# Kernel optimization log

Hardware: AMD Instinct MI355X
Metric: run time of the kernel (lower is better)

The kernel has to match this reference:

```python
import jax, jax.numpy as jnp
import numpy as np

B, N, E, H = 1, 4096, 1024, 16
D = E // H

def setup_inputs() -> dict:
    key = jax.random.key(0)
    k1, k2, k3 = jax.random.split(key, 3)
    s = 1.0 / np.sqrt(E)
    return {
        "x": jax.random.normal(k1, (B, N, E), dtype=jnp.float32),
        "w_qkv": jax.random.normal(k2, (3 * E, E), dtype=jnp.float32) * s,
        "b_qkv": jnp.zeros((3 * E,), dtype=jnp.float32),
        "w_proj": jax.random.normal(k3, (E, E), dtype=jnp.float32) * s,
        "b_proj": jnp.zeros((E,), dtype=jnp.float32),
    }

def reference(x, w_qkv, b_qkv, w_proj, b_proj):
    Bx, Nx, Ex = x.shape
    scale = (Ex // H) ** -0.5
    # torch Linear: x @ W^T + b
    qkv = jnp.einsum('bne,fe->bnf', x, w_qkv) + b_qkv  # [B,N,3E]
    q, k, v = jnp.split(qkv, 3, axis=-1)
    def to_heads(t):
        return t.reshape(Bx, Nx, H, Ex // H).transpose(0, 2, 1, 3)  # b h n d
    q, k, v = to_heads(q), to_heads(k), to_heads(v)
    dots = jnp.einsum('bhnd,bhmd->bhnm', q, k) * scale  # full NxN scores
    attn = jax.nn.softmax(dots, axis=-1)  # dropout=0 (eval)
    out = jnp.einsum('bhnm,bhmd->bhnd', attn, v)
    out = out.transpose(0, 2, 1, 3).reshape(Bx, Nx, Ex)
    return jnp.einsum('bne,fe->bnf', out, w_proj) + b_proj
```

## Files before the change

kernel.cpp:

```cpp
#include <hip/hip_runtime.h>

#define N_TOK 4096
#define E_DIM 1024
#define NH    16
#define HD    64

typedef __bf16 bf16x8 __attribute__((ext_vector_type(8)));
typedef __bf16 bf16x4 __attribute__((ext_vector_type(4)));
typedef float  f32x4  __attribute__((ext_vector_type(4)));
typedef float  f32x16 __attribute__((ext_vector_type(16)));

#define GLOAD16(gsrc, ldst) __builtin_amdgcn_global_load_lds( \
    (const __attribute__((address_space(1))) void*)(gsrc),    \
    (__attribute__((address_space(3))) void*)(ldst), 16, 0, 0)

__device__ __forceinline__ f32x16 zero16() {
    f32x16 z;
#pragma unroll
    for (int i = 0; i < 16; ++i) z[i] = 0.f;
    return z;
}

__device__ __forceinline__ unsigned pk2(float a, float b) {
    union { __bf16 h[2]; unsigned u; } t;
    t.h[0] = (__bf16)a; t.h[1] = (__bf16)b;
    return t.u;
}

__device__ __forceinline__ float fmax3(float a, float b, float c) {
    return fmaxf(fmaxf(a, b), c);
}

__device__ __forceinline__ void load16(const __bf16* __restrict__ p, bf16x8& lo, bf16x8& hi) {
    lo = *(const bf16x8*)p;
    hi = *(const bf16x8*)(p + 8);
}

__device__ __forceinline__ void cvt8(const float* __restrict__ src, __bf16* __restrict__ dst, int i) {
    const float4 a = ((const float4*)src)[i * 2];
    const float4 b = ((const float4*)src)[i * 2 + 1];
    ((bf16x8*)dst)[i] = bf16x8{(__bf16)a.x, (__bf16)a.y, (__bf16)a.z, (__bf16)a.w,
                               (__bf16)b.x, (__bf16)b.y, (__bf16)b.z, (__bf16)b.w};
}

__global__ __launch_bounds__(256) void conv_tri(const float* __restrict__ s1, __bf16* __restrict__ d1, int n1,
                                                const float* __restrict__ s2, __bf16* __restrict__ d2, int n2,
                                                const float* __restrict__ s3, __bf16* __restrict__ d3, int n3) {
    const int i = blockIdx.x * 256 + threadIdx.x;
    if (i < n1)                 cvt8(s1, d1, i);
    else if (i < n1 + n2)       cvt8(s2, d2, i - n1);
    else if (i < n1 + n2 + n3)  cvt8(s3, d3, i - n1 - n2);
}

__global__ __launch_bounds__(256) void conv_pair(const float* __restrict__ s1, __bf16* __restrict__ d1, int n1,
                                                 const float* __restrict__ s2, __bf16* __restrict__ d2, int n2) {
    const int i = blockIdx.x * 256 + threadIdx.x;
    if (i < n1)            cvt8(s1, d1, i);
    else if (i < n1 + n2)  cvt8(s2, d2, i - n1);
}

__global__ __launch_bounds__(256) void conv_bf16(const float* __restrict__ src,
                                                 __bf16* __restrict__ dst, int n8) {
    const int i = blockIdx.x * 256 + threadIdx.x;
    if (i >= n8) return;
    cvt8(src, dst, i);
}

__device__ __forceinline__ void gemm_core(const __bf16* __restrict__ A, const __bf16* __restrict__ B,
                                          const int K, const int rowBase, const int colBase,
                                          __bf16* As, __bf16* Bs, f32x4 (&acc)[4][4]) {
    const int tid = threadIdx.x, lane = tid & 63, wid = tid >> 6;
    const int wm = wid >> 1, wn = wid & 1;
    const int lr = lane & 15, lg = lane >> 4;
    const int lrow = lane >> 2, lcol = (lane & 3) * 8;

    const __bf16* aBase = A + (size_t)(rowBase + wid * 16 + lrow) * K + lcol;
    const __bf16* bBase = B + (size_t)(colBase + wid * 16 + lrow) * K + lcol;
    const size_t row64 = (size_t)64 * K;

    for (int kt = 0; kt < K; kt += 32) {
        __syncthreads();
        GLOAD16(aBase + kt,         As + wid * 512);
        GLOAD16(aBase + row64 + kt, As + 2048 + wid * 512);
        GLOAD16(bBase + kt,         Bs + wid * 512);
        GLOAD16(bBase + row64 + kt, Bs + 2048 + wid * 512);
        __syncthreads();

        bf16x8 af[4], bfr[4];
#pragma unroll
        for (int i = 0; i < 4; ++i) {
            af[i]  = *(const bf16x8*)&As[(wm * 64 + i * 16 + lr) * 32 + lg * 8];
            bfr[i] = *(const bf16x8*)&Bs[(wn * 64 + i * 16 + lr) * 32 + lg * 8];
        }
#pragma unroll
        for (int i = 0; i < 4; ++i)
#pragma unroll
            for (int j = 0; j < 4; ++j)
                acc[i][j] = __builtin_amdgcn_mfma_f32_16x16x32_bf16(af[i], bfr[j], acc[i][j], 0, 0, 0);
    }
}

#define QSCALE 0.180336879f

__global__ __launch_bounds__(256) void qkv_gemm(const __bf16* __restrict__ x,
                                                const __bf16* __restrict__ wqkv,
                                                const float* __restrict__ bqkv,
                                                __bf16* __restrict__ Qb,
                                                __bf16* __restrict__ Kb,
                                                __bf16* __restrict__ VtG) {
    __shared__ __bf16 As[128 * 32];
    __shared__ __bf16 Bs[128 * 32];
    f32x4 acc[4][4];
#pragma unroll
    for (int i = 0; i < 4; ++i)
#pragma unroll
        for (int j = 0; j < 4; ++j)
            acc[i][j] = f32x4{0.f, 0.f, 0.f, 0.f};

    const int lin = blockIdx.y * 32 + blockIdx.x;
    const int swz = (lin & 7) * 96 + (lin >> 3);
    const int tm = swz & 31, tn = swz >> 5;

    gemm_core(x, wqkv, E_DIM, tm * 128, tn * 128, As, Bs, acc);

    const int tid = threadIdx.x;
    const int lane = tid & 63, wid = tid >> 6;
    const int wm = wid >> 1, wn = wid & 1;
    const int lr = lane & 15, lg = lane >> 4;

#pragma unroll
    for (int ni = 0; ni < 4; ++ni) {
        const int f = tn * 128 + wn * 64 + ni * 16 + lr;
        const float bias = bqkv[f];
        const int which = f >> 10;
        const int hh = (f & 1023) >> 6;
        const int dd = f & 63;
        if (which == 2) {
            __bf16* dst = VtG + ((size_t)hh * HD + dd) * N_TOK;
#pragma unroll
            for (int mi = 0; mi < 4; ++mi) {
                const int n0 = tm * 128 + wm * 64 + mi * 16 + lg * 4;
                const int pos = (n0 & ~12) | ((n0 & 4) << 1) | ((n0 & 8) >> 1);
                bf16x4 v;
#pragma unroll
                for (int r = 0; r < 4; ++r) v[r] = (__bf16)(acc[mi][ni][r] + bias);
                *(bf16x4*)&dst[pos] = v;
            }
        } else {
            __bf16* dst = (which == 0) ? Qb : Kb;
            const float sc = (which == 0) ? QSCALE : 1.0f;
#pragma unroll
            for (int mi = 0; mi < 4; ++mi) {
#pragma unroll
                for (int r = 0; r < 4; ++r) {
                    const int n = tm * 128 + wm * 64 + mi * 16 + lg * 4 + r;
                    dst[((size_t)hh * N_TOK + n) * HD + dd] = (__bf16)((acc[mi][ni][r] + bias) * sc);
                }
            }
        }
    }
}

#define QBLK  256
#define KVB   128
#define NTILE (N_TOK / KVB)
#define KST   72
#define VST   136
#define BUFSZ (KVB * KST + HD * VST)

__global__ __launch_bounds__(512, 2) void flash_attn(const __bf16* __restrict__ Qb,
                                                     const __bf16* __restrict__ Kb,
                                                     const __bf16* __restrict__ Vt,
                                                     __bf16* __restrict__ Ob) {
    __shared__ __bf16 smem[2 * BUFSZ];

    const int tid = threadIdx.x, lane = tid & 63, wid = tid >> 6;
    const int lq = lane & 31, hi = lane >> 5;
    const int qg = wid >> 1, hw = wid & 1;

    const int lin = blockIdx.y * 16 + blockIdx.x;
    const int swz = (lin & 7) * 32 + (lin >> 3);
    const int qblk = swz & 15, h = swz >> 4;

    const __bf16* Qh = Qb + (size_t)h * N_TOK * HD;
    const __bf16* Kh = Kb + (size_t)h * N_TOK * HD;
    const __bf16* Vh = Vt + (size_t)h * HD * N_TOK;

    bf16x8 qf[2][4];
#pragma unroll
    for (int g = 0; g < 2; ++g) {
        const size_t qr = (size_t)qblk * QBLK + qg * 64 + g * 32 + lq;
#pragma unroll
        for (int sd = 0; sd < 4; ++sd)
            qf[g][sd] = *(const bf16x8*)&Qh[qr * HD + sd * 16 + hi * 8];
    }

    f32x16 o[2][2], lacc[2];
#pragma unroll
    for (int g = 0; g < 2; ++g) { o[g][0] = zero16(); o[g][1] = zero16(); lacc[g] = zero16(); }
    float m[2] = {-INFINITY, -INFINITY};

    const bf16x8 ones = bf16x8{(__bf16)1.f, (__bf16)1.f, (__bf16)1.f, (__bf16)1.f,
                               (__bf16)1.f, (__bf16)1.f, (__bf16)1.f, (__bf16)1.f};

    const int krow = tid >> 2, kseg = (tid & 3) * 16;
    const int vrow = tid >> 3, vseg = (tid & 7) * 16;
    const __bf16* kSrc = Kh + (size_t)krow * HD + kseg;
    const __bf16* vSrc = Vh + (size_t)vrow * N_TOK + vseg;

    bf16x8 kr0, kr1, vr0, vr1;
    load16(kSrc, kr0, kr1);
    load16(vSrc, vr0, vr1);
    {
        __bf16* Kw = smem;
        __bf16* Vw = smem + KVB * KST;
        *(bf16x8*)&Kw[krow * KST + kseg]     = kr0;
        *(bf16x8*)&Kw[krow * KST + kseg + 8] = kr1;
        *(bf16x8*)&Vw[vrow * VST + vseg]     = vr0;
        *(bf16x8*)&Vw[vrow * VST + vseg + 8] = vr1;
    }

    for (int t = 0; t < NTILE; ++t) {
        const int cur = t & 1;
        const __bf16* Kc = smem + cur * BUFSZ;
        const __bf16* Vc = Kc + KVB * KST;

        if (t + 1 < NTILE) {
            load16(kSrc + (size_t)(t + 1) * KVB * HD, kr0, kr1);
            load16(vSrc + (t + 1) * KVB, vr0, vr1);
        }
        __syncthreads();

        f32x16 s[2][2];
#pragma unroll
        for (int g = 0; g < 2; ++g) { s[g][0] = zero16(); s[g][1] = zero16(); }
        __builtin_amdgcn_s_setprio(1);
#pragma unroll
        for (int sd = 0; sd < 4; ++sd) {
            const bf16x8 kf0 = *(const bf16x8*)&Kc[(hw * 64 + lq) * KST + sd * 16 + hi * 8];
            const bf16x8 kf1 = *(const bf16x8*)&Kc[(hw * 64 + 32 + lq) * KST + sd * 16 + hi * 8];
            s[0][0] = __builtin_amdgcn_mfma_f32_32x32x16_bf16(kf0, qf[0][sd], s[0][0], 0, 0, 0);
            s[0][1] = __builtin_amdgcn_mfma_f32_32x32x16_bf16(kf1, qf[0][sd], s[0][1], 0, 0, 0);
            s[1][0] = __builtin_amdgcn_mfma_f32_32x32x16_bf16(kf0, qf[1][sd], s[1][0], 0, 0, 0);
            s[1][1] = __builtin_amdgcn_mfma_f32_32x32x16_bf16(kf1, qf[1][sd], s[1][1], 0, 0, 0);
        }
        __builtin_amdgcn_s_setprio(0);

        float mx[2];
#pragma unroll
        for (int g = 0; g < 2; ++g) {
            const float t0 = fmax3(s[g][0][0],  s[g][0][1],  s[g][0][2]);
            const float t1 = fmax3(s[g][0][3],  s[g][0][4],  s[g][0][5]);
            const float t2 = fmax3(s[g][0][6],  s[g][0][7],  s[g][0][8]);
            const float t3 = fmax3(s[g][0][9],  s[g][0][10], s[g][0][11]);
            const float t4 = fmax3(s[g][0][12], s[g][0][13], s[g][0][14]);
            const float t5 = fmax3(s[g][1][0],  s[g][1][1],  s[g][1][2]);
            const float t6 = fmax3(s[g][1][3],  s[g][1][4],  s[g][1][5]);
            const float t7 = fmax3(s[g][1][6],  s[g][1][7],  s[g][1][8]);
            const float t8 = fmax3(s[g][1][9],  s[g][1][10], s[g][1][11]);
            const float t9 = fmax3(s[g][1][12], s[g][1][13], s[g][1][14]);
            const float u0 = fmax3(t0, t1, s[g][0][15]);
            const float u1 = fmax3(t2, t3, t4);
            const float u2 = fmax3(t5, t6, s[g][1][15]);
            const float u3 = fmax3(t7, t8, t9);
            float a = fmaxf(fmax3(u0, u1, u2), u3);
            mx[g] = fmaxf(a, __shfl_xor(a, 32));
        }

        if (!__all(mx[0] <= m[0] + 8.f && mx[1] <= m[1] + 8.f)) {
#pragma unroll
            for (int g = 0; g < 2; ++g) {
                const float mn = fmaxf(m[g], mx[g]);
                const float al = __builtin_amdgcn_exp2f(m[g] - mn);
                m[g] = mn;
#pragma unroll
                for (int r = 0; r < 16; ++r) { o[g][0][r] *= al; o[g][1][r] *= al; }
                lacc[g][0] *= al;
            }
        }

#pragma unroll
        for (int w = 0; w < 4; ++w) {
            const int rb = (w & 1) * 8;
            const int half = (w < 2) ? 0 : 1;
            bf16x8 pfv[2];
#pragma unroll
            for (int g = 0; g < 2; ++g) {
                union { unsigned u[4]; bf16x8 v; } pf;
                pf.u[0] = pk2(__builtin_amdgcn_exp2f(s[g][half][rb + 0] - m[g]),
                              __builtin_amdgcn_exp2f(s[g][half][rb + 1] - m[g]));
                pf.u[1] = pk2(__builtin_amdgcn_exp2f(s[g][half][rb + 2] - m[g]),
                              __builtin_amdgcn_exp2f(s[g][half][rb + 3] - m[g]));
                pf.u[2] = pk2(__builtin_amdgcn_exp2f(s[g][half][rb + 4] - m[g]),
                              __builtin_amdgcn_exp2f(s[g][half][rb + 5] - m[g]));
                pf.u[3] = pk2(__builtin_amdgcn_exp2f(s[g][half][rb + 6] - m[g]),
                              __builtin_amdgcn_exp2f(s[g][half][rb + 7] - m[g]));
                pfv[g] = pf.v;
            }

            const bf16x8 vf0 = *(const bf16x8*)&Vc[lq * VST + hw * 64 + w * 16 + hi * 8];
            const bf16x8 vf1 = *(const bf16x8*)&Vc[(32 + lq) * VST + hw * 64 + w * 16 + hi * 8];
            __builtin_amdgcn_s_setprio(1);
            o[0][0] = __builtin_amdgcn_mfma_f32_32x32x16_bf16(vf0, pfv[0], o[0][0], 0, 0, 0);
            o[0][1] = __builtin_amdgcn_mfma_f32_32x32x16_bf16(vf1, pfv[0], o[0][1], 0, 0, 0);
            o[1][0] = __builtin_amdgcn_mfma_f32_32x32x16_bf16(vf0, pfv[1], o[1][0], 0, 0, 0);
            o[1][1] = __builtin_amdgcn_mfma_f32_32x32x16_bf16(vf1, pfv[1], o[1][1], 0, 0, 0);
            lacc[0] = __builtin_amdgcn_mfma_f32_32x32x16_bf16(ones, pfv[0], lacc[0], 0, 0, 0);
            lacc[1] = __builtin_amdgcn_mfma_f32_32x32x16_bf16(ones, pfv[1], lacc[1], 0, 0, 0);
            __builtin_amdgcn_s_setprio(0);
        }

        if (t + 1 < NTILE) {
            __bf16* Kw = smem + (cur ^ 1) * BUFSZ;
            __bf16* Vw = Kw + KVB * KST;
            *(bf16x8*)&Kw[krow * KST + kseg]     = kr0;
            *(bf16x8*)&Kw[krow * KST + kseg + 8] = kr1;
            *(bf16x8*)&Vw[vrow * VST + vseg]     = vr0;
            *(bf16x8*)&Vw[vrow * VST + vseg + 8] = vr1;
        }
    }

    __syncthreads();
    float* scratch = (float*)smem;
    if (hw == 1) {
#pragma unroll
        for (int g = 0; g < 2; ++g) {
            float* po = scratch + (qg * 2 + g) * 2080;
#pragma unroll
            for (int r = 0; r < 16; ++r) {
                const int d0 = (r & 3) + 8 * (r >> 2) + 4 * hi;
                po[lq * 65 + d0]      = o[g][0][r];
                po[lq * 65 + 32 + d0] = o[g][1][r];
            }
            if (hi == 0) {
                float* plm = scratch + 16640 + (qg * 2 + g) * 64;
                plm[lq * 2] = lacc[g][0]; plm[lq * 2 + 1] = m[g];
            }
        }
    }
    __syncthreads();
    if (hw == 0) {
#pragma unroll
        for (int g = 0; g < 2; ++g) {
            float* po  = scratch + (qg * 2 + g) * 2080;
            float* plm = scratch + 16640 + (qg * 2 + g) * 64;
            const float l1 = plm[lq * 2], m1 = plm[lq * 2 + 1];
            const float M  = fmaxf(m[g], m1);
            const float a0 = __builtin_amdgcn_exp2f(m[g] - M);
            const float a1 = __builtin_amdgcn_exp2f(m1 - M);
            const float inv = 1.0f / (lacc[g][0] * a0 + l1 * a1);
            const size_t qr = (size_t)qblk * QBLK + qg * 64 + g * 32 + lq;
            __bf16* obase = &Ob[qr * E_DIM + h * HD];
#pragma unroll
            for (int grp = 0; grp < 4; ++grp) {
                bf16x4 v0, v1;
#pragma unroll
                for (int c = 0; c < 4; ++c) {
                    const int r = grp * 4 + c;
                    const int d0 = c + 8 * grp + 4 * hi;
                    v0[c] = (__bf16)((o[g][0][r] * a0 + po[lq * 65 + d0]      * a1) * inv);
                    v1[c] = (__bf16)((o[g][1][r] * a0 + po[lq * 65 + 32 + d0] * a1) * inv);
                }
                *(bf16x4*)&obase[grp * 8 + hi * 4]      = v0;
                *(bf16x4*)&obase[32 + grp * 8 + hi * 4] = v1;
            }
        }
    }
}

__global__ __launch_bounds__(256) void proj_gemm(const __bf16* __restrict__ Ob,
                                                 const __bf16* __restrict__ wp,
                                                 const float* __restrict__ bp,
                                                 float* __restrict__ out) {
    __shared__ __bf16 As[64 * 32];
    __shared__ __bf16 Bs[128 * 32];
    f32x4 acc[2][4];
#pragma unroll
    for (int i = 0; i < 2; ++i)
#pragma unroll
        for (int j = 0; j < 4; ++j)
            acc[i][j] = f32x4{0.f, 0.f, 0.f, 0.f};

    const int lin = blockIdx.y * 64 + blockIdx.x;
    const int swz = (lin & 7) * 64 + (lin >> 3);
    const int tm = swz & 63, tn = swz >> 6;

    const int tid = threadIdx.x, lane = tid & 63, wid = tid >> 6;
    const int wm = wid >> 1, wn = wid & 1;
    const int lr = lane & 15, lg = lane >> 4;
    const int lrow = lane >> 2, lcol = (lane & 3) * 8;

    const __bf16* aBase = Ob + (size_t)(tm * 64 + wid * 16 + lrow) * E_DIM + lcol;
    const __bf16* bBase = wp + (size_t)(tn * 128 + wid * 16 + lrow) * E_DIM + lcol;
    const size_t row64 = (size_t)64 * E_DIM;

    for (int kt = 0; kt < E_DIM; kt += 32) {
        __syncthreads();
        GLOAD16(aBase + kt,         As + wid * 512);
        GLOAD16(bBase + kt,         Bs + wid * 512);
        GLOAD16(bBase + row64 + kt, Bs + 2048 + wid * 512);
        __syncthreads();

        bf16x8 af[2], bfr[4];
#pragma unroll
        for (int i = 0; i < 2; ++i)
            af[i]  = *(const bf16x8*)&As[(wm * 32 + i * 16 + lr) * 32 + lg * 8];
#pragma unroll
        for (int j = 0; j < 4; ++j)
            bfr[j] = *(const bf16x8*)&Bs[(wn * 64 + j * 16 + lr) * 32 + lg * 8];
#pragma unroll
        for (int i = 0; i < 2; ++i)
#pragma unroll
            for (int j = 0; j < 4; ++j)
                acc[i][j] = __builtin_amdgcn_mfma_f32_16x16x32_bf16(af[i], bfr[j], acc[i][j], 0, 0, 0);
    }

#pragma unroll
    for (int ni = 0; ni < 4; ++ni) {
        const int f = tn * 128 + wn * 64 + ni * 16 + lr;
        const float bias = bp[f];
#pragma unroll
        for (int mi = 0; mi < 2; ++mi) {
#pragma unroll
            for (int r = 0; r < 4; ++r) {
                const int n = tm * 64 + wm * 32 + mi * 16 + lg * 4 + r;
                out[(size_t)n * E_DIM + f] = acc[mi][ni][r] + bias;
            }
        }
    }
}

extern "C" void kernel_launch(void* const* d_in, const int* in_sizes, int n_in,
                              void* d_out, int out_size, void* d_ws, size_t ws_size,
                              hipStream_t stream) {
    const float* x     = (const float*)d_in[0];
    const float* wqkv  = (const float*)d_in[1];
    const float* bqkv  = (const float*)d_in[2];
    const float* wproj = (const float*)d_in[3];
    const float* bproj = (const float*)d_in[4];
    float* out = (float*)d_out;

    const size_t headElems = (size_t)NH * N_TOK * HD;
    __bf16* Qb   = (__bf16*)d_ws;
    __bf16* Kb   = Qb + headElems;
    __bf16* VtG  = Kb + headElems;
    __bf16* ObXb = VtG + headElems;
    __bf16* Wb   = ObXb + headElems;

    const int n1 = N_TOK * E_DIM / 8;
    const int n2 = 3 * E_DIM * E_DIM / 8;
    const int n3 = E_DIM * E_DIM / 8;

    const size_t needBytes = (4 * headElems + (size_t)(3 + 1) * E_DIM * E_DIM) * sizeof(__bf16);
    const bool sep = ws_size >= needBytes;
    __bf16* Wp = sep ? (Wb + (size_t)3 * E_DIM * E_DIM) : Wb;

    if (sep) {
        conv_tri<<<(n1 + n2 + n3 + 255) / 256, 256, 0, stream>>>(x, ObXb, n1, wqkv, Wb, n2, wproj, Wp, n3);
    } else {
        conv_pair<<<(n1 + n2 + 255) / 256, 256, 0, stream>>>(x, ObXb, n1, wqkv, Wb, n2);
    }

    qkv_gemm<<<dim3(N_TOK / 128, 3 * E_DIM / 128), 256, 0, stream>>>(ObXb, Wb, bqkv, Qb, Kb, VtG);

    if (!sep) {
        conv_bf16<<<(n3 + 255) / 256, 256, 0, stream>>>(wproj, Wp, n3);
    }

    flash_attn<<<dim3(N_TOK / QBLK, NH), 512, 0, stream>>>(Qb, Kb, VtG, ObXb);

    proj_gemm<<<dim3(N_TOK / 64, E_DIM / 128), 256, 0, stream>>>(ObXb, Wp, bproj, out);
}
```

Baseline: 153.2 us.

## Load K/V fragments directly from global memory instead of LDS staging

Removes the double-buffered LDS staging of K and V tiles and the per-tile __syncthreads in the flash attention loop. Each wave now reads its K and V MFMA fragments straight from global memory into registers, so there is no barrier and no LDS round-trip. The cost is that the four query-group waves sharing the same K/V rows now fetch them redundantly through cache, and without software prefetch the loads are exposed latency. There is also added register pressure under launch_bounds(512,2).

```diff
diff --git a/kernel.cpp b/kernel.cpp
--- a/kernel.cpp
+++ b/kernel.cpp
@@ -29,11 +29,6 @@
 
 __device__ __forceinline__ float fmax3(float a, float b, float c) {
     return fmaxf(fmaxf(a, b), c);
-}
-
-__device__ __forceinline__ void load16(const __bf16* __restrict__ p, bf16x8& lo, bf16x8& hi) {
-    lo = *(const bf16x8*)p;
-    hi = *(const bf16x8*)(p + 8);
 }
 
 __device__ __forceinline__ void cvt8(const float* __restrict__ src, __bf16* __restrict__ dst, int i) {
@@ -164,15 +159,12 @@
 #define QBLK  256
 #define KVB   128
 #define NTILE (N_TOK / KVB)
-#define KST   72
-#define VST   136
-#define BUFSZ (KVB * KST + HD * VST)
 
 __global__ __launch_bounds__(512, 2) void flash_attn(const __bf16* __restrict__ Qb,
                                                      const __bf16* __restrict__ Kb,
                                                      const __bf16* __restrict__ Vt,
                                                      __bf16* __restrict__ Ob) {
-    __shared__ __bf16 smem[2 * BUFSZ];
+    __shared__ float scratch[17152];
 
     const int tid = threadIdx.x, lane = tid & 63, wid = tid >> 6;
     const int lq = lane & 31, hi = lane >> 5;
@@ -203,33 +195,18 @@
     const bf16x8 ones = bf16x8{(__bf16)1.f, (__bf16)1.f, (__bf16)1.f, (__bf16)1.f,
                                (__bf16)1.f, (__bf16)1.f, (__bf16)1.f, (__bf16)1.f};
 
-    const int krow = tid >> 2, kseg = (tid & 3) * 16;
-    const int vrow = tid >> 3, vseg = (tid & 7) * 16;
-    const __bf16* kSrc = Kh + (size_t)krow * HD + kseg;
-    const __bf16* vSrc = Vh + (size_t)vrow * N_TOK + vseg;
-
-    bf16x8 kr0, kr1, vr0, vr1;
-    load16(kSrc, kr0, kr1);
-    load16(vSrc, vr0, vr1);
-    {
-        __bf16* Kw = smem;
-        __bf16* Vw = smem + KVB * KST;
-        *(bf16x8*)&Kw[krow * KST + kseg]     = kr0;
-        *(bf16x8*)&Kw[krow * KST + kseg + 8] = kr1;
-        *(bf16x8*)&Vw[vrow * VST + vseg]     = vr0;
-        *(bf16x8*)&Vw[vrow * VST + vseg + 8] = vr1;
-    }
+    const __bf16* kRow0 = Kh + (size_t)(hw * 64 + lq) * HD;
+    const __bf16* kRow1 = kRow0 + (size_t)32 * HD;
+    const __bf16* vRow0 = Vh + (size_t)lq * N_TOK + hw * 64;
+    const __bf16* vRow1 = vRow0 + (size_t)32 * N_TOK;
 
     for (int t = 0; t < NTILE; ++t) {
-        const int cur = t & 1;
-        const __bf16* Kc = smem + cur * BUFSZ;
-        const __bf16* Vc = Kc + KVB * KST;
-
-        if (t + 1 < NTILE) {
-            load16(kSrc + (size_t)(t + 1) * KVB * HD, kr0, kr1);
-            load16(vSrc + (t + 1) * KVB, vr0, vr1);
-        }
-        __syncthreads();
+        bf16x8 kf0[4], kf1[4];
+#pragma unroll
+        for (int sd = 0; sd < 4; ++sd) {
+            kf0[sd] = *(const bf16x8*)(kRow0 + sd * 16 + hi * 8);
+            kf1[sd] = *(const bf16x8*)(kRow1 + sd * 16 + hi * 8);
+        }
 
         f32x16 s[2][2];
 #pragma unroll
@@ -237,14 +214,19 @@
         __builtin_amdgcn_s_setprio(1);
 #pragma unroll
         for (int sd = 0; sd < 4; ++sd) {
-            const bf16x8 kf0 = *(const bf16x8*)&Kc[(hw * 64 + lq) * KST + sd * 16 + hi * 8];
-            const bf16x8 kf1 = *(const bf16x8*)&Kc[(hw * 64 + 32 + lq) * KST + sd * 16 + hi * 8];
-            s[0][0] = __builtin_amdgcn_mfma_f32_32x32x16_bf16(kf0, qf[0][sd], s[0][0], 0, 0, 0);
-            s[0][1] = __builtin_amdgcn_mfma_f32_32x32x16_bf16(kf1, qf[0][sd], s[0][1], 0, 0, 0);
-            s[1][0] = __builtin_amdgcn_mfma_f32_32x32x16_bf16(kf0, qf[1][sd], s[1][0], 0, 0, 0);
-            s[1][1] = __builtin_amdgcn_mfma_f32_32x32x16_bf16(kf1, qf[1][sd], s[1][1], 0, 0, 0);
+            s[0][0] = __builtin_amdgcn_mfma_f32_32x32x16_bf16(kf0[sd], qf[0][sd], s[0][0], 0, 0, 0);
+            s[0][1] = __builtin_amdgcn_mfma_f32_32x32x16_bf16(kf1[sd], qf[0][sd], s[0][1], 0, 0, 0);
+            s[1][0] = __builtin_amdgcn_mfma_f32_32x32x16_bf16(kf0[sd], qf[1][sd], s[1][0], 0, 0, 0);
+            s[1][1] = __builtin_amdgcn_mfma_f32_32x32x16_bf16(kf1[sd], qf[1][sd], s[1][1], 0, 0, 0);
         }
         __builtin_amdgcn_s_setprio(0);
+
+        bf16x8 vf0[4], vf1[4];
+#pragma unroll
+        for (int w = 0; w < 4; ++w) {
+            vf0[w] = *(const bf16x8*)(vRow0 + w * 16 + hi * 8);
+            vf1[w] = *(const bf16x8*)(vRow1 + w * 16 + hi * 8);
+        }
 
         float mx[2];
 #pragma unroll
@@ -298,30 +280,22 @@
                 pfv[g] = pf.v;
             }
 
-            const bf16x8 vf0 = *(const bf16x8*)&Vc[lq * VST + hw * 64 + w * 16 + hi * 8];
-            const bf16x8 vf1 = *(const bf16x8*)&Vc[(32 + lq) * VST + hw * 64 + w * 16 + hi * 8];
             __builtin_amdgcn_s_setprio(1);
-            o[0][0] = __builtin_amdgcn_mfma_f32_32x32x16_bf16(vf0, pfv[0], o[0][0], 0, 0, 0);
-            o[0][1] = __builtin_amdgcn_mfma_f32_32x32x16_bf16(vf1, pfv[0], o[0][1], 0, 0, 0);
-            o[1][0] = __builtin_amdgcn_mfma_f32_32x32x16_bf16(vf0, pfv[1], o[1][0], 0, 0, 0);
-            o[1][1] = __builtin_amdgcn_mfma_f32_32x32x16_bf16(vf1, pfv[1], o[1][1], 0, 0, 0);
+            o[0][0] = __builtin_amdgcn_mfma_f32_32x32x16_bf16(vf0[w], pfv[0], o[0][0], 0, 0, 0);
+            o[0][1] = __builtin_amdgcn_mfma_f32_32x32x16_bf16(vf1[w], pfv[0], o[0][1], 0, 0, 0);
+            o[1][0] = __builtin_amdgcn_mfma_f32_32x32x16_bf16(vf0[w], pfv[1], o[1][0], 0, 0, 0);
+            o[1][1] = __builtin_amdgcn_mfma_f32_32x32x16_bf16(vf1[w], pfv[1], o[1][1], 0, 0, 0);
             lacc[0] = __builtin_amdgcn_mfma_f32_32x32x16_bf16(ones, pfv[0], lacc[0], 0, 0, 0);
             lacc[1] = __builtin_amdgcn_mfma_f32_32x32x16_bf16(ones, pfv[1], lacc[1], 0, 0, 0);
             __builtin_amdgcn_s_setprio(0);
         }
 
-        if (t + 1 < NTILE) {
-            __bf16* Kw = smem + (cur ^ 1) * BUFSZ;
-            __bf16* Vw = Kw + KVB * KST;
-            *(bf16x8*)&Kw[krow * KST + kseg]     = kr0;
-            *(bf16x8*)&Kw[krow * KST + kseg + 8] = kr1;
-            *(bf16x8*)&Vw[vrow * VST + vseg]     = vr0;
-            *(bf16x8*)&Vw[vrow * VST + vseg + 8] = vr1;
-        }
-    }
-
-    __syncthreads();
-    float* scratch = (float*)smem;
+        kRow0 += (size_t)KVB * HD;
+        kRow1 += (size_t)KVB * HD;
+        vRow0 += KVB;
+        vRow1 += KVB;
+    }
+
     if (hw == 1) {
 #pragma unroll
         for (int g = 0; g < 2; ++g) {
```

After: 186.6 us. 1.22x slower.

## Double KV tile to 256 and interleave half-tile prefetch with compute

Applied to the files above, without the earlier changes.

Raises the flash-attention KV tile from 128 to 256 keys, so the loop runs half as many iterations and block barriers. Each tile is processed in two 128-key halves. The prefetched register data for the first half is written to LDS, and the second half's global load is issued between the two compute halves, overlapping loads with MFMA work. The double-buffered LDS footprint roughly doubles to about 141KB per block. That likely cuts resident blocks per CU from the two requested by launch bounds to one, reducing occupancy and latency hiding.

```diff
diff --git a/kernel.cpp b/kernel.cpp
--- a/kernel.cpp
+++ b/kernel.cpp
@@ -162,10 +162,10 @@
 }
 
 #define QBLK  256
-#define KVB   128
+#define KVB   256
 #define NTILE (N_TOK / KVB)
 #define KST   72
-#define VST   136
+#define VST   264
 #define BUFSZ (KVB * KST + HD * VST)
 
 __global__ __launch_bounds__(512, 2) void flash_attn(const __bf16* __restrict__ Qb,
@@ -203,42 +203,15 @@
     const bf16x8 ones = bf16x8{(__bf16)1.f, (__bf16)1.f, (__bf16)1.f, (__bf16)1.f,
                                (__bf16)1.f, (__bf16)1.f, (__bf16)1.f, (__bf16)1.f};
 
-    const int krow = tid >> 2, kseg = (tid & 3) * 16;
-    const int vrow = tid >> 3, vseg = (tid & 7) * 16;
-    const __bf16* kSrc = Kh + (size_t)krow * HD + kseg;
-    const __bf16* vSrc = Vh + (size_t)vrow * N_TOK + vseg;
-
-    bf16x8 kr0, kr1, vr0, vr1;
-    load16(kSrc, kr0, kr1);
-    load16(vSrc, vr0, vr1);
-    {
-        __bf16* Kw = smem;
-        __bf16* Vw = smem + KVB * KST;
-        *(bf16x8*)&Kw[krow * KST + kseg]     = kr0;
-        *(bf16x8*)&Kw[krow * KST + kseg + 8] = kr1;
-        *(bf16x8*)&Vw[vrow * VST + vseg]     = vr0;
-        *(bf16x8*)&Vw[vrow * VST + vseg + 8] = vr1;
-    }
-
-    for (int t = 0; t < NTILE; ++t) {
-        const int cur = t & 1;
-        const __bf16* Kc = smem + cur * BUFSZ;
-        const __bf16* Vc = Kc + KVB * KST;
-
-        if (t + 1 < NTILE) {
-            load16(kSrc + (size_t)(t + 1) * KVB * HD, kr0, kr1);
-            load16(vSrc + (t + 1) * KVB, vr0, vr1);
-        }
-        __syncthreads();
-
+    auto computeHalf = [&](const __bf16* Kc, const __bf16* Vc, const int base) {
         f32x16 s[2][2];
 #pragma unroll
         for (int g = 0; g < 2; ++g) { s[g][0] = zero16(); s[g][1] = zero16(); }
         __builtin_amdgcn_s_setprio(1);
 #pragma unroll
         for (int sd = 0; sd < 4; ++sd) {
-            const bf16x8 kf0 = *(const bf16x8*)&Kc[(hw * 64 + lq) * KST + sd * 16 + hi * 8];
-            const bf16x8 kf1 = *(const bf16x8*)&Kc[(hw * 64 + 32 + lq) * KST + sd * 16 + hi * 8];
+            const bf16x8 kf0 = *(const bf16x8*)&Kc[(base + hw * 64 + lq) * KST + sd * 16 + hi * 8];
+            const bf16x8 kf1 = *(const bf16x8*)&Kc[(base + hw * 64 + 32 + lq) * KST + sd * 16 + hi * 8];
             s[0][0] = __builtin_amdgcn_mfma_f32_32x32x16_bf16(kf0, qf[0][sd], s[0][0], 0, 0, 0);
             s[0][1] = __builtin_amdgcn_mfma_f32_32x32x16_bf16(kf1, qf[0][sd], s[0][1], 0, 0, 0);
             s[1][0] = __builtin_amdgcn_mfma_f32_32x32x16_bf16(kf0, qf[1][sd], s[1][0], 0, 0, 0);
@@ -298,8 +271,8 @@
                 pfv[g] = pf.v;
             }
 
-            const bf16x8 vf0 = *(const bf16x8*)&Vc[lq * VST + hw * 64 + w * 16 + hi * 8];
-            const bf16x8 vf1 = *(const bf16x8*)&Vc[(32 + lq) * VST + hw * 64 + w * 16 + hi * 8];
+            const bf16x8 vf0 = *(const bf16x8*)&Vc[lq * VST + base + hw * 64 + w * 16 + hi * 8];
+            const bf16x8 vf1 = *(const bf16x8*)&Vc[(32 + lq) * VST + base + hw * 64 + w * 16 + hi * 8];
             __builtin_amdgcn_s_setprio(1);
             o[0][0] = __builtin_amdgcn_mfma_f32_32x32x16_bf16(vf0, pfv[0], o[0][0], 0, 0, 0);
             o[0][1] = __builtin_amdgcn_mfma_f32_32x32x16_bf16(vf1, pfv[0], o[0][1], 0, 0, 0);
@@ -309,14 +282,67 @@
             lacc[1] = __builtin_amdgcn_mfma_f32_32x32x16_bf16(ones, pfv[1], lacc[1], 0, 0, 0);
             __builtin_amdgcn_s_setprio(0);
         }
-
-        if (t + 1 < NTILE) {
+    };
+
+    const int krow = tid >> 2, kseg = (tid & 3) * 16;
+    const int vrow = tid >> 3, vseg = (tid & 7) * 16;
+    const __bf16* kSrc = Kh + (size_t)krow * HD + kseg;
+    const __bf16* vSrc = Vh + (size_t)vrow * N_TOK + vseg;
+    const int kw = krow * KST + kseg;
+    const int vw = vrow * VST + vseg;
+
+    bf16x8 kr0, kr1, vr0, vr1;
+    {
+        __bf16* Kw = smem;
+        __bf16* Vw = smem + KVB * KST;
+        load16(kSrc, kr0, kr1);
+        load16(vSrc, vr0, vr1);
+        *(bf16x8*)&Kw[kw]     = kr0;
+        *(bf16x8*)&Kw[kw + 8] = kr1;
+        *(bf16x8*)&Vw[vw]     = vr0;
+        *(bf16x8*)&Vw[vw + 8] = vr1;
+        load16(kSrc + (size_t)128 * HD, kr0, kr1);
+        load16(vSrc + 128, vr0, vr1);
+        *(bf16x8*)&Kw[128 * KST + kw] = kr0;
+        *(bf16x8*)&Kw[128 * KST + kw + 8] = kr1;
+        *(bf16x8*)&Vw[vw + 128]     = vr0;
+        *(bf16x8*)&Vw[vw + 128 + 8] = vr1;
+    }
+
+    for (int t = 0; t < NTILE; ++t) {
+        const int cur = t & 1;
+        const __bf16* Kc = smem + cur * BUFSZ;
+        const __bf16* Vc = Kc + KVB * KST;
+        const bool pre = (t + 1 < NTILE);
+
+        if (pre) {
+            load16(kSrc + (size_t)(t + 1) * KVB * HD, kr0, kr1);
+            load16(vSrc + (t + 1) * KVB, vr0, vr1);
+        }
+        __syncthreads();
+
+        computeHalf(Kc, Vc, 0);
+
+        if (pre) {
             __bf16* Kw = smem + (cur ^ 1) * BUFSZ;
             __bf16* Vw = Kw + KVB * KST;
-            *(bf16x8*)&Kw[krow * KST + kseg]     = kr0;
-            *(bf16x8*)&Kw[krow * KST + kseg + 8] = kr1;
-            *(bf16x8*)&Vw[vrow * VST + vseg]     = vr0;
-            *(bf16x8*)&Vw[vrow * VST + vseg + 8] = vr1;
+            *(bf16x8*)&Kw[kw]     = kr0;
+            *(bf16x8*)&Kw[kw + 8] = kr1;
+            *(bf16x8*)&Vw[vw]     = vr0;
+            *(bf16x8*)&Vw[vw + 8] = vr1;
+            load16(kSrc + (size_t)((t + 1) * KVB + 128) * HD, kr0, kr1);
+            load16(vSrc + (t + 1) * KVB + 128, vr0, vr1);
+        }
+
+        computeHalf(Kc, Vc, 128);
+
+        if (pre) {
+            __bf16* Kw = smem + (cur ^ 1) * BUFSZ;
+            __bf16* Vw = Kw + KVB * KST;
+            *(bf16x8*)&Kw[128 * KST + kw]     = kr0;
+            *(bf16x8*)&Kw[128 * KST + kw + 8] = kr1;
+            *(bf16x8*)&Vw[vw + 128]     = vr0;
+            *(bf16x8*)&Vw[vw + 128 + 8] = vr1;
         }
     }
 
```

After: 154.0 us. Within noise of the previous version (+0.5%).
